# Kernel optimization log

Hardware: AMD Instinct MI355X
Metric: run time of the kernel (lower is better)

Reference implementation:

```python
import jax, jax.numpy as jnp
import numpy as np

TAU = 2.0        # spikingjelly LIFNode default tau
VTH = 1.0        # v_threshold
ALPHA = 2.0      # ATan surrogate alpha
NUM_HEADS = 8
N_WIN = 8
TOPK = 4


@jax.custom_vjp
def atan_heaviside(x):
    # spike = H(v - v_th), with ATan surrogate gradient
    return (x >= 0.0).astype(x.dtype)

def _ah_fwd(x):
    return atan_heaviside(x), x

def _ah_bwd(x, g):
    half_pi_alpha = np.float32(np.pi / 2.0 * ALPHA)
    return (g * (ALPHA / 2.0) / (1.0 + (half_pi_alpha * x) ** 2),)

atan_heaviside.defvjp(_ah_fwd, _ah_bwd)


def lif(x):
    """Multi-step LIF over leading time dim. decay_input=True, v_reset=0, detach_reset."""
    def step(v, xt):
        v = v + (xt - v) / TAU                      # charge
        s = atan_heaviside(v - VTH)                 # fire
        v = v * (1.0 - jax.lax.stop_gradient(s))    # hard reset (detached)
        return v, s
    _, spikes = jax.lax.scan(step, jnp.zeros_like(x[0]), x)
    return spikes


def setup_inputs() -> dict:
    key = jax.random.key(0)
    k1, k2, k3, k4, k5 = jax.random.split(key, 5)
    T, B, L, C = 4, 4, 1024, 256
    x = jax.random.normal(k1, (T, B, L, C), dtype=jnp.float32)
    w_qkv = jax.random.normal(k2, (C, 3 * C), dtype=jnp.float32) * (C ** -0.5)
    b_qkv = jax.random.normal(k3, (3 * C,), dtype=jnp.float32) * 0.02
    w_proj = jax.random.normal(k4, (C, C), dtype=jnp.float32) * (C ** -0.5)
    b_proj = jax.random.normal(k5, (C,), dtype=jnp.float32) * 0.02
    return {"x": x, "w_qkv": w_qkv, "b_qkv": b_qkv, "w_proj": w_proj, "b_proj": b_proj}


def reference(x, w_qkv, b_qkv, w_proj, b_proj):
    T, B, L, C = x.shape
    hd = C // NUM_HEADS
    win = L // N_WIN
    scale = hd ** -0.5

    # --- region-level routing (on raw input summed over time) ---
    xs = x.sum(axis=0).reshape(B, N_WIN, win, C)
    region = xs.sum(axis=2)                                  # [B, n_win, C]
    attn_r = jnp.einsum('bnc,bmc->bnm', region, region) * (C ** -0.5)
    _, idx = jax.lax.top_k(attn_r, TOPK)                     # [B, n_win, topk] int32

    # --- qkv + LIF spiking ---
    qkv = x @ w_qkv + b_qkv                                  # [T,B,L,3C]
    q, k, v = jnp.split(qkv, 3, axis=-1)
    q, k, v = lif(q), lif(k), lif(v)
    q = q.reshape(T, B, N_WIN, win, NUM_HEADS, hd)
    k = k.reshape(T, B, N_WIN, win, NUM_HEADS, hd)
    v = v.reshape(T, B, N_WIN, win, NUM_HEADS, hd)

    # --- gather routed KV windows (vectorized; topk-major concat like torch.cat) ---
    b_idx = jnp.arange(B)[:, None, None]                     # [B,1,1]
    k_g = k[:, b_idx, idx].reshape(T, B, N_WIN, TOPK * win, NUM_HEADS, hd)
    v_g = v[:, b_idx, idx].reshape(T, B, N_WIN, TOPK * win, NUM_HEADS, hd)

    # --- windowed attention over gathered keys ---
    attn = jnp.einsum('tbnqhd,tbnkhd->tbnhqk', q, k_g) * scale
    attn = jax.nn.softmax(attn, axis=-1)
    out = jnp.einsum('tbnhqk,tbnkhd->tbnqhd', attn, v_g).reshape(T, B, L, C)

    out = lif(out @ w_proj + b_proj)
    return out
```

## Files before the change

### kernel.cpp

```cpp
#include <hip/hip_runtime.h>
#include <cstdint>
#include <cstddef>

#define TT 4
#define BB 4
#define LL 1024
#define CC 256
#define HH 8
#define HD 32
#define NWIN 8
#define WIN 128
#define TOPKN 4
#define C3 768

__global__ __launch_bounds__(64) void region_kernel(const float* __restrict__ x,
                                                    float* __restrict__ region) {
    int bn = blockIdx.x;
    int b = bn >> 3, n = bn & 7;
    int c = blockIdx.y * 64 + threadIdx.x;
    float tot = 0.0f;
    for (int r = 0; r < WIN; ++r) {
        int l = n * WIN + r;
        float s = 0.0f;
        for (int t = 0; t < TT; ++t) {
            s += x[(((size_t)t * BB + b) * LL + l) * CC + c];
        }
        tot += s;
    }
    region[(size_t)bn * CC + c] = tot;
}

__global__ __launch_bounds__(64) void route_kernel(const float* __restrict__ region,
                                                   int* __restrict__ idx) {
    int b = blockIdx.x;
    __shared__ float reg[NWIN][CC];
    __shared__ float attn_r[NWIN][NWIN];
    int tid = threadIdx.x;
    for (int e = tid; e < NWIN * CC; e += 64)
        reg[e >> 8][e & 255] = region[(size_t)b * NWIN * CC + e];
    __syncthreads();
    int n = tid >> 3, m = tid & 7;
    float s = 0.0f;
    for (int c = 0; c < CC; ++c) s += reg[n][c] * reg[m][c];
    attn_r[n][m] = s * 0.0625f;
    __syncthreads();
    if (tid < NWIN) {
        float vals[NWIN];
        for (int m2 = 0; m2 < NWIN; ++m2) vals[m2] = attn_r[tid][m2];
        for (int kk = 0; kk < TOPKN; ++kk) {
            int bi = 0; float bv = vals[0];
            for (int m2 = 1; m2 < NWIN; ++m2) {
                if (vals[m2] > bv) { bv = vals[m2]; bi = m2; }
            }
            idx[(b * NWIN + tid) * TOPKN + kk] = bi;
            vals[bi] = -INFINITY;
        }
    }
}

__global__ __launch_bounds__(256, 3) void gemm_bias128(const float* __restrict__ A,
                                                       const float* __restrict__ W,
                                                       const float* __restrict__ bias,
                                                       float* __restrict__ C,
                                                       int M, int N, int K) {
    const int BM = 128, BN = 128, BK = 16, TM = 8;
    __shared__ float As[BK][BM + 4];
    __shared__ float Bs[BK][136];
    int tid = threadIdx.x;
    int tx = tid & 15, ty = tid >> 4;
    int bm = blockIdx.x * BM, bn = blockIdx.y * BN;
    float acc[TM][8] = {};
    for (int k0 = 0; k0 < K; k0 += BK) {
#pragma unroll
        for (int it = 0; it < 2; ++it) {
            int i = it * 256 + tid;
            int row = i >> 2, kc = (i & 3) * 4;
            float4 v = *(const float4*)(A + (size_t)(bm + row) * K + k0 + kc);
            As[kc + 0][row] = v.x; As[kc + 1][row] = v.y;
            As[kc + 2][row] = v.z; As[kc + 3][row] = v.w;
        }
#pragma unroll
        for (int it = 0; it < 2; ++it) {
            int i = it * 256 + tid;
            int kr = i >> 5, nc = (i & 31) * 4;
            float4 v = *(const float4*)(W + (size_t)(k0 + kr) * N + bn + nc);
            *(float4*)&Bs[kr][nc] = v;
        }
        __syncthreads();
#pragma unroll
        for (int kk = 0; kk < BK; ++kk) {
            float a[TM], bb[8];
            const float4* ap = (const float4*)&As[kk][ty * TM];
            float4 a0 = ap[0], a1 = ap[1];
            a[0]=a0.x; a[1]=a0.y; a[2]=a0.z; a[3]=a0.w;
            a[4]=a1.x; a[5]=a1.y; a[6]=a1.z; a[7]=a1.w;
            float4 b0 = *(const float4*)&Bs[kk][tx * 4];
            float4 b1 = *(const float4*)&Bs[kk][64 + tx * 4];
            bb[0]=b0.x; bb[1]=b0.y; bb[2]=b0.z; bb[3]=b0.w;
            bb[4]=b1.x; bb[5]=b1.y; bb[6]=b1.z; bb[7]=b1.w;
#pragma unroll
            for (int i = 0; i < TM; ++i)
#pragma unroll
                for (int j = 0; j < 8; ++j)
                    acc[i][j] = fmaf(a[i], bb[j], acc[i][j]);
        }
        __syncthreads();
    }
#pragma unroll
    for (int i = 0; i < TM; ++i) {
        int row = bm + ty * TM + i;
        int col0 = bn + tx * 4;
        int col1 = bn + 64 + tx * 4;
        float4 o0 = make_float4(acc[i][0] + bias[col0 + 0], acc[i][1] + bias[col0 + 1],
                                acc[i][2] + bias[col0 + 2], acc[i][3] + bias[col0 + 3]);
        float4 o1 = make_float4(acc[i][4] + bias[col1 + 0], acc[i][5] + bias[col1 + 1],
                                acc[i][6] + bias[col1 + 2], acc[i][7] + bias[col1 + 3]);
        *(float4*)&C[(size_t)row * N + col0] = o0;
        *(float4*)&C[(size_t)row * N + col1] = o1;
    }
}

__global__ __launch_bounds__(256, 4) void gemm_bias64(const float* __restrict__ A,
                                                      const float* __restrict__ W,
                                                      const float* __restrict__ bias,
                                                      float* __restrict__ C,
                                                      int M, int N, int K) {
    const int BM = 64, BN = 64, BK = 16;
    __shared__ float As[BK][BM + 4];
    __shared__ float Bs[BK][72];
    int tid = threadIdx.x;
    int tx = tid & 15, ty = tid >> 4;
    int bm = blockIdx.x * BM, bn = blockIdx.y * BN;
    float acc[4][4] = {};
    for (int k0 = 0; k0 < K; k0 += BK) {
        {
            int row = tid >> 2, kc = (tid & 3) * 4;
            float4 v = *(const float4*)(A + (size_t)(bm + row) * K + k0 + kc);
            As[kc + 0][row] = v.x; As[kc + 1][row] = v.y;
            As[kc + 2][row] = v.z; As[kc + 3][row] = v.w;
        }
        {
            int kr = tid >> 4, nc = (tid & 15) * 4;
            float4 v = *(const float4*)(W + (size_t)(k0 + kr) * N + bn + nc);
            *(float4*)&Bs[kr][nc] = v;
        }
        __syncthreads();
#pragma unroll
        for (int kk = 0; kk < BK; ++kk) {
            float4 av = *(const float4*)&As[kk][ty * 4];
            float4 bv = *(const float4*)&Bs[kk][tx * 4];
            float a[4] = {av.x, av.y, av.z, av.w};
            float bb[4] = {bv.x, bv.y, bv.z, bv.w};
#pragma unroll
            for (int i = 0; i < 4; ++i)
#pragma unroll
                for (int j = 0; j < 4; ++j)
                    acc[i][j] = fmaf(a[i], bb[j], acc[i][j]);
        }
        __syncthreads();
    }
#pragma unroll
    for (int i = 0; i < 4; ++i) {
        int row = bm + ty * 4 + i;
        int col = bn + tx * 4;
        float4 o = make_float4(acc[i][0] + bias[col + 0], acc[i][1] + bias[col + 1],
                               acc[i][2] + bias[col + 2], acc[i][3] + bias[col + 3]);
        *(float4*)&C[(size_t)row * N + col] = o;
    }
}

__global__ __launch_bounds__(256) void lif_kernel(const float* src, float* dst, size_t stride) {
    size_t i = ((size_t)blockIdx.x * blockDim.x + threadIdx.x) * 4;
    float v[4] = {0.f, 0.f, 0.f, 0.f};
    for (int t = 0; t < TT; ++t) {
        float4 xv4 = *(const float4*)(src + (size_t)t * stride + i);
        float xv[4] = {xv4.x, xv4.y, xv4.z, xv4.w};
        float sp[4];
#pragma unroll
        for (int j = 0; j < 4; ++j) {
            v[j] = v[j] + (xv[j] - v[j]) * 0.5f;
            bool fire = (v[j] >= 1.0f);
            sp[j] = fire ? 1.0f : 0.0f;
            v[j] = fire ? 0.0f : v[j];
        }
        *(float4*)(dst + (size_t)t * stride + i) = make_float4(sp[0], sp[1], sp[2], sp[3]);
    }
}

__global__ __launch_bounds__(192) void lif_pack_kernel(float* __restrict__ qkv,
                                                       uint32_t* __restrict__ pk) {
    int row = blockIdx.x;
    int tid = threadIdx.x;
    int c = tid * 4;
    int wid = tid >> 6;
    int lane = tid & 63;
    const size_t stride = (size_t)BB * LL * C3;
    float* base = qkv + (size_t)row * C3 + c;

    float v[4] = {0.f, 0.f, 0.f, 0.f};
    for (int t = 0; t < TT; ++t) {
        float4 xv4 = *(const float4*)(base + (size_t)t * stride);
        float xv[4] = {xv4.x, xv4.y, xv4.z, xv4.w};
        bool fire[4];
        float sp[4];
#pragma unroll
        for (int j = 0; j < 4; ++j) {
            v[j] = v[j] + (xv[j] - v[j]) * 0.5f;
            fire[j] = (v[j] >= 1.0f);
            sp[j] = fire[j] ? 1.0f : 0.0f;
            v[j] = fire[j] ? 0.0f : v[j];
        }
        if (c >= 512)
            *(float4*)(base + (size_t)t * stride) = make_float4(sp[0], sp[1], sp[2], sp[3]);
        unsigned long long B0 = __ballot(fire[0]);
        unsigned long long B1 = __ballot(fire[1]);
        unsigned long long B2 = __ballot(fire[2]);
        unsigned long long B3 = __ballot(fire[3]);
        if (lane < 8 && wid < 2) {
            uint32_t word = ((uint32_t)(B0 >> (8 * lane)) & 0xFFu)
                          | (((uint32_t)(B1 >> (8 * lane)) & 0xFFu) << 8)
                          | (((uint32_t)(B2 >> (8 * lane)) & 0xFFu) << 16)
                          | (((uint32_t)(B3 >> (8 * lane)) & 0xFFu) << 24);
            pk[((size_t)t * BB * LL + row) * 16 + wid * 8 + lane] = word;
        }
    }
}

__global__ __launch_bounds__(256) void attn_sm(const uint32_t* __restrict__ pk,
                                               const int* __restrict__ idxws,
                                               float2* __restrict__ amz) {
    int bid = blockIdx.x;
    int hp = bid & 3, n = (bid >> 2) & 7, b = (bid >> 5) & 3, t = bid >> 7;
    __shared__ uint32_t kbs[2][512];
    int tid = threadIdx.x;
    int q = tid & 127, h = tid >> 7;
    int lbase = (t * BB + b) * LL;

    const int* ip = idxws + (b * NWIN + n) * TOPKN;
    int s0r = ip[0], s1r = ip[1], s2r = ip[2], s3r = ip[3];

#pragma unroll 4
    for (int e = tid; e < 1024; e += 256) {
        int hh = e >> 9, kk = e & 511;
        int w = kk >> 7;
        int sw = (w == 0) ? s0r : (w == 1) ? s1r : (w == 2) ? s2r : s3r;
        int row = sw * WIN + (kk & 127);
        kbs[hh][kk] = pk[(size_t)(lbase + row) * 16 + 8 + hp * 2 + hh];
    }
    uint32_t qw = pk[(size_t)(lbase + n * WIN + q) * 16 + hp * 2 + h];
    __syncthreads();

    const float ALPHA_SC = 0.17677669529663687f;
    const uint4* kb4 = (const uint4*)kbs[h];
    int smax = 0;
#pragma unroll 8
    for (int k4 = 0; k4 < 128; ++k4) {
        uint4 w4 = kb4[k4];
        smax = max(smax, __popc(qw & w4.x));
        smax = max(smax, __popc(qw & w4.y));
        smax = max(smax, __popc(qw & w4.z));
        smax = max(smax, __popc(qw & w4.w));
    }
    float am = __fmul_rn((float)smax, ALPHA_SC);
    float Z = 0.0f;
#pragma unroll 4
    for (int k4 = 0; k4 < 128; ++k4) {
        uint4 w4 = kb4[k4];
        Z += expf(__fsub_rn(__fmul_rn((float)__popc(qw & w4.x), ALPHA_SC), am));
        Z += expf(__fsub_rn(__fmul_rn((float)__popc(qw & w4.y), ALPHA_SC), am));
        Z += expf(__fsub_rn(__fmul_rn((float)__popc(qw & w4.z), ALPHA_SC), am));
        Z += expf(__fsub_rn(__fmul_rn((float)__popc(qw & w4.w), ALPHA_SC), am));
    }
    amz[(size_t)(lbase + n * WIN + q) * HH + hp * 2 + h] = make_float2(am, Z);
}

__global__ __launch_bounds__(256, 4) void attn_pv(const float* __restrict__ spk,
                                                  const uint32_t* __restrict__ pk,
                                                  const int* __restrict__ idxws,
                                                  const float2* __restrict__ amz,
                                                  float* __restrict__ out) {
    int bid = blockIdx.x;
    int h = bid & 1, hp = (bid >> 1) & 3, n = (bid >> 3) & 7, b = (bid >> 6) & 3, t = bid >> 8;
    __shared__ __align__(16) float Vlds[2][64][32];
    __shared__ float ptab[33][WIN];
    __shared__ __align__(16) uint32_t kbs[4 * WIN];
    int tid = threadIdx.x;
    int qg = tid & 63, dh = tid >> 6;
    int lbase = (t * BB + b) * LL;

    const int* ip = idxws + (b * NWIN + n) * TOPKN;
    int s0r = ip[0], s1r = ip[1], s2r = ip[2], s3r = ip[3];

#pragma unroll 2
    for (int e = tid; e < 512; e += 256) {
        int w = e >> 7;
        int sw = (w == 0) ? s0r : (w == 1) ? s1r : (w == 2) ? s2r : s3r;
        int row = sw * WIN + (e & 127);
        kbs[e] = pk[(size_t)(lbase + row) * 16 + 8 + hp * 2 + h];
    }
    uint32_t qw0 = pk[(size_t)(lbase + n * WIN + qg) * 16 + hp * 2 + h];
    uint32_t qw1 = pk[(size_t)(lbase + n * WIN + qg + 64) * 16 + hp * 2 + h];

    const float* vsrc = spk + (size_t)lbase * C3 + 512 + hp * 64 + h * 32
                        + (size_t)(tid >> 3) * C3 + (tid & 7) * 4;
    int wvoff = (tid >> 6) * 1024;

#define STAGE_HALF(hw_)                                                              \
    do {                                                                             \
        int hw = (hw_);                                                              \
        int ww = hw >> 1;                                                            \
        int sw = (ww == 0) ? s0r : (ww == 1) ? s1r : (ww == 2) ? s2r : s3r;          \
        const float* src = vsrc + (size_t)sw * (WIN * C3)                            \
                                + (size_t)(hw & 1) * 64 * C3;                        \
        char* lb = (char*)(&Vlds[hw & 1][0][0]) + wvoff;                             \
        __builtin_amdgcn_global_load_lds(                                            \
            (const __attribute__((address_space(1))) void*)src,                      \
            (__attribute__((address_space(3))) void*)lb, 16, 0, 0);                  \
        __builtin_amdgcn_global_load_lds(                                            \
            (const __attribute__((address_space(1))) void*)(src + 32 * C3),          \
            (__attribute__((address_space(3))) void*)(lb + 4096), 16, 0, 0);         \
    } while (0)

    STAGE_HALF(0);
    STAGE_HALF(1);

    {
        if (tid < 128) {
            float2 az = amz[(size_t)(lbase + n * WIN + tid) * HH + hp * 2 + h];
            const float ALPHA_SC = 0.17677669529663687f;
            for (int s = 0; s <= 32; ++s)
                ptab[s][tid] = expf(__fsub_rn(__fmul_rn((float)s, ALPHA_SC), az.x)) / az.y;
        }
    }

    float acc0[8], acc1[8];
#pragma unroll
    for (int d = 0; d < 8; ++d) { acc0[d] = 0.0f; acc1[d] = 0.0f; }

    asm volatile("s_waitcnt vmcnt(2)" ::: "memory");
    __syncthreads();

    const uint4* kb4 = (const uint4*)kbs;

#pragma unroll
    for (int hw = 0; hw < 8; ++hw) {
        const uint4* kw4 = kb4 + hw * 16;
        const float* vb = &Vlds[hw & 1][0][dh * 8];
#pragma unroll 2
        for (int g = 0; g < 16; ++g) {
            uint4 kw = kw4[g];
            const float* pr = vb + g * 128;
#pragma unroll
            for (int jp = 0; jp < 2; ++jp) {
                uint32_t ka = (jp == 0) ? kw.x : kw.z;
                uint32_t kb_ = (jp == 0) ? kw.y : kw.w;
                float Pa0 = ptab[__popc(qw0 & ka)][qg];
                float Pa1 = ptab[__popc(qw1 & ka)][qg + 64];
                float Pb0 = ptab[__popc(qw0 & kb_)][qg];
                float Pb1 = ptab[__popc(qw1 & kb_)][qg + 64];
                const float4* va = (const float4*)(pr + jp * 64);
                const float4* vbp = (const float4*)(pr + jp * 64 + 32);
                float4 a0 = va[0], a1 = va[1];
                float4 b0 = vbp[0], b1 = vbp[1];
                acc0[0] = fmaf(Pa0, a0.x, acc0[0]);  acc1[0] = fmaf(Pa1, a0.x, acc1[0]);
                acc0[1] = fmaf(Pa0, a0.y, acc0[1]);  acc1[1] = fmaf(Pa1, a0.y, acc1[1]);
                acc0[2] = fmaf(Pa0, a0.z, acc0[2]);  acc1[2] = fmaf(Pa1, a0.z, acc1[2]);
                acc0[3] = fmaf(Pa0, a0.w, acc0[3]);  acc1[3] = fmaf(Pa1, a0.w, acc1[3]);
                acc0[4] = fmaf(Pa0, a1.x, acc0[4]);  acc1[4] = fmaf(Pa1, a1.x, acc1[4]);
                acc0[5] = fmaf(Pa0, a1.y, acc0[5]);  acc1[5] = fmaf(Pa1, a1.y, acc1[5]);
                acc0[6] = fmaf(Pa0, a1.z, acc0[6]);  acc1[6] = fmaf(Pa1, a1.z, acc1[6]);
                acc0[7] = fmaf(Pa0, a1.w, acc0[7]);  acc1[7] = fmaf(Pa1, a1.w, acc1[7]);
                acc0[0] = fmaf(Pb0, b0.x, acc0[0]);  acc1[0] = fmaf(Pb1, b0.x, acc1[0]);
                acc0[1] = fmaf(Pb0, b0.y, acc0[1]);  acc1[1] = fmaf(Pb1, b0.y, acc1[1]);
                acc0[2] = fmaf(Pb0, b0.z, acc0[2]);  acc1[2] = fmaf(Pb1, b0.z, acc1[2]);
                acc0[3] = fmaf(Pb0, b0.w, acc0[3]);  acc1[3] = fmaf(Pb1, b0.w, acc1[3]);
                acc0[4] = fmaf(Pb0, b1.x, acc0[4]);  acc1[4] = fmaf(Pb1, b1.x, acc1[4]);
                acc0[5] = fmaf(Pb0, b1.y, acc0[5]);  acc1[5] = fmaf(Pb1, b1.y, acc1[5]);
                acc0[6] = fmaf(Pb0, b1.z, acc0[6]);  acc1[6] = fmaf(Pb1, b1.z, acc1[6]);
                acc0[7] = fmaf(Pb0, b1.w, acc0[7]);  acc1[7] = fmaf(Pb1, b1.w, acc1[7]);
            }
        }

        if (hw < 7) {
            __syncthreads();
            if (hw < 6) {
                STAGE_HALF(hw + 2);
                asm volatile("s_waitcnt vmcnt(2)" ::: "memory");
            } else {
                asm volatile("s_waitcnt vmcnt(0)" ::: "memory");
            }
            __syncthreads();
        }
    }
#undef STAGE_HALF

    size_t ob0 = (size_t)(lbase + n * WIN + qg) * CC + (hp * 2 + h) * 32 + dh * 8;
    size_t ob1 = ob0 + (size_t)64 * CC;
    *(float4*)&out[ob0]     = make_float4(acc0[0], acc0[1], acc0[2], acc0[3]);
    *(float4*)&out[ob0 + 4] = make_float4(acc0[4], acc0[5], acc0[6], acc0[7]);
    *(float4*)&out[ob1]     = make_float4(acc1[0], acc1[1], acc1[2], acc1[3]);
    *(float4*)&out[ob1 + 4] = make_float4(acc1[4], acc1[5], acc1[6], acc1[7]);
}

extern "C" void kernel_launch(void* const* d_in, const int* in_sizes, int n_in,
                              void* d_out, int out_size, void* d_ws, size_t ws_size,
                              hipStream_t stream) {
    const float* x      = (const float*)d_in[0];
    const float* w_qkv  = (const float*)d_in[1];
    const float* b_qkv  = (const float*)d_in[2];
    const float* w_proj = (const float*)d_in[3];
    const float* b_proj = (const float*)d_in[4];
    float* ws = (float*)d_ws;

    float* qkv      = ws;
    float* attn_out = ws + 12582912;
    float* proj     = ws + 16777216;
    uint32_t* pkb   = (uint32_t*)proj;
    float* region   = ws + 20971520;
    int*   idxp     = (int*)(ws + 20979712);
    float2* amzp    = (float2*)(ws + 20979840);
    float* outp     = (float*)d_out;

    region_kernel<<<dim3(BB * NWIN, 4), dim3(64), 0, stream>>>(x, region);
    route_kernel<<<dim3(BB), dim3(64), 0, stream>>>(region, idxp);
    gemm_bias128<<<dim3(128, 6), dim3(256), 0, stream>>>(x, w_qkv, b_qkv, qkv,
                                                         TT * BB * LL, C3, CC);
    lif_pack_kernel<<<dim3(BB * LL), dim3(192), 0, stream>>>(qkv, pkb);
    attn_sm<<<dim3(TT * BB * NWIN * 4), dim3(256), 0, stream>>>(pkb, idxp, amzp);
    attn_pv<<<dim3(TT * BB * NWIN * 4 * 2), dim3(256), 0, stream>>>(qkv, pkb, idxp, amzp, attn_out);
    gemm_bias64<<<dim3(256, 4), dim3(256), 0, stream>>>(attn_out, w_proj, b_proj, proj,
                                                        TT * BB * LL, CC, CC);
    lif_kernel<<<dim3(1024), dim3(256), 0, stream>>>(proj, outp, (size_t)BB * LL * CC);
}
```

Baseline: 261.4 us.

## Fuse softmax statistics kernel into attn_pv and use table lookups for normalizer

Removes the separate attn_sm kernel and computes the per-query row max and softmax normalizer inside attn_pv from the already staged K bitmasks. The exp values are tabulated once per possible popcount and reused to sum Z, replacing 512 expf calls per query with table lookups. This drops one launch and the amz round trip through global memory. In exchange only 128 of 256 threads do the max/Z work while the V loads are in flight, and some __syncthreads become raw s_barrier with manual waitcnt.

Measured after the change: 245.9 us. 1.06x faster.

```diff
diff --git a/kernel.cpp b/kernel.cpp
--- a/kernel.cpp
+++ b/kernel.cpp
@@ -226,58 +226,9 @@
     }
 }
 
-__global__ __launch_bounds__(256) void attn_sm(const uint32_t* __restrict__ pk,
-                                               const int* __restrict__ idxws,
-                                               float2* __restrict__ amz) {
-    int bid = blockIdx.x;
-    int hp = bid & 3, n = (bid >> 2) & 7, b = (bid >> 5) & 3, t = bid >> 7;
-    __shared__ uint32_t kbs[2][512];
-    int tid = threadIdx.x;
-    int q = tid & 127, h = tid >> 7;
-    int lbase = (t * BB + b) * LL;
-
-    const int* ip = idxws + (b * NWIN + n) * TOPKN;
-    int s0r = ip[0], s1r = ip[1], s2r = ip[2], s3r = ip[3];
-
-#pragma unroll 4
-    for (int e = tid; e < 1024; e += 256) {
-        int hh = e >> 9, kk = e & 511;
-        int w = kk >> 7;
-        int sw = (w == 0) ? s0r : (w == 1) ? s1r : (w == 2) ? s2r : s3r;
-        int row = sw * WIN + (kk & 127);
-        kbs[hh][kk] = pk[(size_t)(lbase + row) * 16 + 8 + hp * 2 + hh];
-    }
-    uint32_t qw = pk[(size_t)(lbase + n * WIN + q) * 16 + hp * 2 + h];
-    __syncthreads();
-
-    const float ALPHA_SC = 0.17677669529663687f;
-    const uint4* kb4 = (const uint4*)kbs[h];
-    int smax = 0;
-#pragma unroll 8
-    for (int k4 = 0; k4 < 128; ++k4) {
-        uint4 w4 = kb4[k4];
-        smax = max(smax, __popc(qw & w4.x));
-        smax = max(smax, __popc(qw & w4.y));
-        smax = max(smax, __popc(qw & w4.z));
-        smax = max(smax, __popc(qw & w4.w));
-    }
-    float am = __fmul_rn((float)smax, ALPHA_SC);
-    float Z = 0.0f;
-#pragma unroll 4
-    for (int k4 = 0; k4 < 128; ++k4) {
-        uint4 w4 = kb4[k4];
-        Z += expf(__fsub_rn(__fmul_rn((float)__popc(qw & w4.x), ALPHA_SC), am));
-        Z += expf(__fsub_rn(__fmul_rn((float)__popc(qw & w4.y), ALPHA_SC), am));
-        Z += expf(__fsub_rn(__fmul_rn((float)__popc(qw & w4.z), ALPHA_SC), am));
-        Z += expf(__fsub_rn(__fmul_rn((float)__popc(qw & w4.w), ALPHA_SC), am));
-    }
-    amz[(size_t)(lbase + n * WIN + q) * HH + hp * 2 + h] = make_float2(am, Z);
-}
-
 __global__ __launch_bounds__(256, 4) void attn_pv(const float* __restrict__ spk,
                                                   const uint32_t* __restrict__ pk,
                                                   const int* __restrict__ idxws,
-                                                  const float2* __restrict__ amz,
                                                   float* __restrict__ out) {
     int bid = blockIdx.x;
     int h = bid & 1, hp = (bid >> 1) & 3, n = (bid >> 3) & 7, b = (bid >> 6) & 3, t = bid >> 8;
@@ -324,23 +275,45 @@
     STAGE_HALF(0);
     STAGE_HALF(1);
 
-    {
-        if (tid < 128) {
-            float2 az = amz[(size_t)(lbase + n * WIN + tid) * HH + hp * 2 + h];
-            const float ALPHA_SC = 0.17677669529663687f;
-            for (int s = 0; s <= 32; ++s)
-                ptab[s][tid] = expf(__fsub_rn(__fmul_rn((float)s, ALPHA_SC), az.x)) / az.y;
-        }
+    asm volatile("s_waitcnt lgkmcnt(0)" ::: "memory");
+    __builtin_amdgcn_s_barrier();
+
+    const float ALPHA_SC = 0.17677669529663687f;
+    const uint4* kb4 = (const uint4*)kbs;
+    if (tid < 128) {
+        uint32_t qwt = (tid & 64) ? qw1 : qw0;
+        int smax = 0;
+#pragma unroll 8
+        for (int k4 = 0; k4 < 128; ++k4) {
+            uint4 w4 = kb4[k4];
+            smax = max(smax, __popc(qwt & w4.x));
+            smax = max(smax, __popc(qwt & w4.y));
+            smax = max(smax, __popc(qwt & w4.z));
+            smax = max(smax, __popc(qwt & w4.w));
+        }
+        float am = __fmul_rn((float)smax, ALPHA_SC);
+        for (int s = 0; s <= 32; ++s)
+            ptab[s][tid] = expf(__fsub_rn(__fmul_rn((float)s, ALPHA_SC), am));
+        float Z = 0.0f;
+#pragma unroll 4
+        for (int k4 = 0; k4 < 128; ++k4) {
+            uint4 w4 = kb4[k4];
+            Z += ptab[__popc(qwt & w4.x)][tid];
+            Z += ptab[__popc(qwt & w4.y)][tid];
+            Z += ptab[__popc(qwt & w4.z)][tid];
+            Z += ptab[__popc(qwt & w4.w)][tid];
+        }
+        for (int s = 0; s <= 32; ++s)
+            ptab[s][tid] = ptab[s][tid] / Z;
     }
 
     float acc0[8], acc1[8];
 #pragma unroll
     for (int d = 0; d < 8; ++d) { acc0[d] = 0.0f; acc1[d] = 0.0f; }
 
+    asm volatile("s_waitcnt lgkmcnt(0)" ::: "memory");
     asm volatile("s_waitcnt vmcnt(2)" ::: "memory");
-    __syncthreads();
-
-    const uint4* kb4 = (const uint4*)kbs;
+    __builtin_amdgcn_s_barrier();
 
 #pragma unroll
     for (int hw = 0; hw < 8; ++hw) {
@@ -382,14 +355,14 @@
         }
 
         if (hw < 7) {
-            __syncthreads();
+            __builtin_amdgcn_s_barrier();
             if (hw < 6) {
                 STAGE_HALF(hw + 2);
                 asm volatile("s_waitcnt vmcnt(2)" ::: "memory");
             } else {
                 asm volatile("s_waitcnt vmcnt(0)" ::: "memory");
             }
-            __syncthreads();
+            __builtin_amdgcn_s_barrier();
         }
     }
 #undef STAGE_HALF
@@ -418,7 +391,6 @@
     uint32_t* pkb   = (uint32_t*)proj;
     float* region   = ws + 20971520;
     int*   idxp     = (int*)(ws + 20979712);
-    float2* amzp    = (float2*)(ws + 20979840);
     float* outp     = (float*)d_out;
 
     region_kernel<<<dim3(BB * NWIN, 4), dim3(64), 0, stream>>>(x, region);
@@ -426,8 +398,7 @@
     gemm_bias128<<<dim3(128, 6), dim3(256), 0, stream>>>(x, w_qkv, b_qkv, qkv,
                                                          TT * BB * LL, C3, CC);
     lif_pack_kernel<<<dim3(BB * LL), dim3(192), 0, stream>>>(qkv, pkb);
-    attn_sm<<<dim3(TT * BB * NWIN * 4), dim3(256), 0, stream>>>(pkb, idxp, amzp);
-    attn_pv<<<dim3(TT * BB * NWIN * 4 * 2), dim3(256), 0, stream>>>(qkv, pkb, idxp, amzp, attn_out);
+    attn_pv<<<dim3(TT * BB * NWIN * 4 * 2), dim3(256), 0, stream>>>(qkv, pkb, idxp, attn_out);
     gemm_bias64<<<dim3(256, 4), dim3(256), 0, stream>>>(attn_out, w_proj, b_proj, proj,
                                                         TT * BB * LL, CC, CC);
     lif_kernel<<<dim3(1024), dim3(256), 0, stream>>>(proj, outp, (size_t)BB * LL * CC);
```
